# Performance work log

Measured on AMD Instinct MI355X. Metric: run time of the kernel, lower is better.

## Reference

```python
import jax, jax.numpy as jnp
import numpy as np

N_ATOMS = 8192
N_PAIR = 131072
F = 128
N_HEAD = 8
FH = F // N_HEAD            # 16
DEGREES = [1, 2, 3]
N_DEG = len(DEGREES)
REPEATS = np.array([2 * l + 1 for l in DEGREES])  # [3,5,7]
M_TOT = int(REPEATS.sum())  # 15
K_RBF = 32
H_FILT = 64
FILT_OUT = 2 * N_DEG * F    # 768


def setup_inputs() -> dict:
    key = jax.random.key(0)
    ks = jax.random.split(key, 12)
    x = jax.random.normal(ks[0], (N_ATOMS, F), dtype=jnp.float32)
    rbf_ij = jax.random.uniform(ks[1], (N_PAIR, K_RBF), dtype=jnp.float32)
    sph_ij = jax.random.normal(ks[2], (N_PAIR, M_TOT), dtype=jnp.float32)
    phi_r_cut = jax.random.uniform(ks[3], (N_PAIR,), dtype=jnp.float32)
    idx_i = jnp.sort(jax.random.randint(ks[4], (N_PAIR,), 0, N_ATOMS))
    idx_j = jax.random.randint(ks[5], (N_PAIR,), 0, N_ATOMS)
    pair_mask = jnp.ones((N_PAIR,), dtype=jnp.float32)
    # params (lecun-normal-ish scaling)
    W_Q = jax.random.normal(ks[6], (N_DEG, N_HEAD, FH, FH), dtype=jnp.float32) / np.sqrt(FH)
    W_K = jax.random.normal(ks[7], (N_DEG, N_HEAD, FH, FH), dtype=jnp.float32) / np.sqrt(FH)
    a = jax.random.normal(ks[8], (N_DEG, N_HEAD, 2 * FH), dtype=jnp.float32) / np.sqrt(2 * FH)
    mlp_w1 = jax.random.normal(ks[9], (K_RBF, H_FILT), dtype=jnp.float32) / np.sqrt(K_RBF)
    mlp_b1 = jnp.zeros((H_FILT,), dtype=jnp.float32)
    mlp_w2 = jax.random.normal(ks[10], (H_FILT, FILT_OUT), dtype=jnp.float32) / np.sqrt(H_FILT)
    mlp_b2 = jnp.zeros((FILT_OUT,), dtype=jnp.float32)
    return {"x": x, "rbf_ij": rbf_ij, "sph_ij": sph_ij, "phi_r_cut": phi_r_cut,
            "idx_i": idx_i, "idx_j": idx_j, "pair_mask": pair_mask,
            "W_Q": W_Q, "W_K": W_K, "a": a,
            "mlp_w1": mlp_w1, "mlp_b1": mlp_b1, "mlp_w2": mlp_w2, "mlp_b2": mlp_b2}


def reference(x, rbf_ij, sph_ij, phi_r_cut, idx_i, idx_j, pair_mask,
              W_Q, W_K, a, mlp_w1, mlp_b1, mlp_w2, mlp_b2):
    n = x.shape[0]
    x_head = x.reshape(n, N_HEAD, FH)                       # (n, h, fh)
    # per-atom, per-degree, per-head linear maps
    Q = jnp.einsum('dhij,nhj->ndhi', W_Q, x_head)           # (n, d, h, fh)
    K = jnp.einsum('dhij,nhj->ndhi', W_K, x_head)
    m4 = pair_mask[:, None, None, None]
    Q_i = Q[idx_i] * m4                                     # (p, d, h, fh)
    K_j = K[idx_j] * m4
    QK = jnp.concatenate((Q_i, K_j), axis=-1)               # (p, d, h, 2fh)
    # radial filter MLP
    h1 = jax.nn.silu(rbf_ij @ mlp_w1 + mlp_b1)
    W_ij = (h1 @ mlp_w2 + mlp_b2).reshape(-1, N_DEG, N_HEAD, 2 * FH)
    W_ij = W_ij * phi_r_cut[:, None, None, None]
    # attention logits (non-softmax)
    alpha = jnp.sum(QK * W_ij * a[None], axis=-1)           # (p, d, h)
    alpha = jnp.repeat(alpha, REPEATS, axis=1, total_repeat_length=M_TOT)  # (p, m, h)
    alpha = alpha / jnp.sqrt(jnp.float32(FH))               # att_scale
    # outer product with spherical harmonics + scatter
    x_j = x_head[idx_j] * pair_mask[:, None, None]          # (p, h, fh)
    z = alpha[..., None] * (sph_ij[:, :, None, None] * x_j[:, None, :, :])  # (p, m, h, fh)
    z = z.reshape(z.shape[0], M_TOT, F)                     # (p, m, F)
    return jax.ops.segment_sum(z, idx_i, num_segments=n)    # (n, m, F)
```

## Files before the change

kernel.cpp:

```cpp
#include <hip/hip_runtime.h>
#include <hip/hip_bf16.h>

#define N_ATOMS 8192
#define N_PAIR  131072
#define F       128
#define N_HEAD  8
#define FH      16
#define N_DEG   3
#define M_TOT   15
#define K_RBF   32
#define H_FILT  64
#define FILT_OUT 768
#define NDH     24

typedef __attribute__((ext_vector_type(8))) unsigned short u16x8;

__device__ __forceinline__ float bf2f(unsigned short u) {
    return __uint_as_float(((unsigned)u) << 16);
}
__device__ __forceinline__ unsigned short f2bfbits(float f) {
    __hip_bfloat16 b = __float2bfloat16(f);
    return *reinterpret_cast<unsigned short*>(&b);
}

__global__ void k_seg(const int* __restrict__ idx_i, int* __restrict__ row_start) {
    int p = blockIdx.x * 256 + threadIdx.x;
    if (p >= N_PAIR) return;
    int ii = idx_i[p];
    int prev = (p == 0) ? -1 : idx_i[p - 1];
    for (int a = prev + 1; a <= ii; ++a) row_start[a] = p;
    if (p == N_PAIR - 1) {
        for (int a = ii + 1; a <= N_ATOMS; ++a) row_start[a] = N_PAIR;
    }
}

__global__ void k_zero(int* __restrict__ counts, int* __restrict__ cnt2) {
    int t = blockIdx.x * 256 + threadIdx.x;
    if (t < N_ATOMS) { counts[t] = 0; cnt2[t] = 0; }
}

__global__ void k_hist(const int* __restrict__ idx_j, int* __restrict__ counts) {
    int p = blockIdx.x * 256 + threadIdx.x;
    if (p < N_PAIR) atomicAdd(&counts[idx_j[p]], 1);
}

__global__ __launch_bounds__(1024) void k_scan(const int* __restrict__ counts,
                                               int* __restrict__ offsets) {
    __shared__ int ts[1024];
    int tid = threadIdx.x;
    int base = tid * 8;
    int v[8]; int tot = 0;
    #pragma unroll
    for (int q = 0; q < 8; ++q) { v[q] = counts[base + q]; tot += v[q]; }
    ts[tid] = tot; __syncthreads();
    for (int off = 1; off < 1024; off <<= 1) {
        int t2 = (tid >= off) ? ts[tid - off] : 0;
        __syncthreads();
        ts[tid] += t2;
        __syncthreads();
    }
    int excl = ts[tid] - tot;
    #pragma unroll
    for (int q = 0; q < 8; ++q) { offsets[base + q] = excl; excl += v[q]; }
    if (tid == 1023) offsets[N_ATOMS] = ts[1023];
}

__global__ void k_place(const int* __restrict__ idx_j, const int* __restrict__ offsets,
                        int* __restrict__ cnt2, int* __restrict__ sorted,
                        int* __restrict__ rank) {
    int p = blockIdx.x * 256 + threadIdx.x;
    if (p < N_PAIR) {
        int j = idx_j[p];
        int pos = offsets[j] + atomicAdd(&cnt2[j], 1);
        sorted[pos] = p;
        rank[p] = pos;
    }
}

__global__ __launch_bounds__(256) void k_wc(
    const float* __restrict__ WQ, const float* __restrict__ WK,
    const float* __restrict__ avec, const float* __restrict__ W2,
    const float* __restrict__ b2,
    float* __restrict__ Wc, float* __restrict__ bc)
{
    int bx = blockIdx.x;
    int side = bx / NDH, dh = bx % NDH;
    int d = dh >> 3, h = dh & 7;
    int colbase = d * 256 + h * 32 + side * 16;
    const float* W = (side == 0) ? WQ : WK;
    __shared__ float w2s[64][16];
    __shared__ float ws[16][16];
    __shared__ float as[16];
    __shared__ float b2s[16];
    int tid = threadIdx.x;
    for (int e = tid; e < 64 * 16; e += 256)
        w2s[e >> 4][e & 15] = W2[(e >> 4) * FILT_OUT + colbase + (e & 15)];
    if (tid < 16 * 16) ws[tid >> 4][tid & 15] = W[((d * 8 + h) * 16) * 16 + tid];
    if (tid < 16) { as[tid] = avec[dh * 32 + side * 16 + tid]; b2s[tid] = b2[colbase + tid]; }
    __syncthreads();
    for (int o = tid; o < 64 * 16; o += 256) {
        int k = o >> 4, j = o & 15;
        float s = 0.f;
        #pragma unroll
        for (int c = 0; c < 16; ++c) s += w2s[k][c] * as[c] * ws[c][j];
        Wc[((size_t)bx * 64 + k) * 16 + j] = s;
    }
    if (tid < 16) {
        float s = 0.f;
        #pragma unroll
        for (int c = 0; c < 16; ++c) s += b2s[c] * as[c] * ws[c][tid];
        bc[bx * 16 + tid] = s;
    }
}

__global__ __launch_bounds__(256) void k_gfused(
    const float* __restrict__ x, const float* __restrict__ Wc,
    const float* __restrict__ bc,
    __hip_bfloat16* __restrict__ Gq, __hip_bfloat16* __restrict__ Gk,
    float* __restrict__ bq, float* __restrict__ bk)
{
    int bx = blockIdx.x;
    int by = blockIdx.y;
    int side = by / NDH, dh = by % NDH;
    int h = dh & 7;
    int n0 = bx * 64;
    __shared__ float xh[64][17];
    __shared__ float bcs[16];
    int tid = threadIdx.x;
    for (int e = tid; e < 64 * 16; e += 256)
        xh[e >> 4][e & 15] = x[(size_t)(n0 + (e >> 4)) * F + h * 16 + (e & 15)];
    if (tid < 16) bcs[tid] = bc[by * 16 + tid];
    int k = tid & 63, wv = tid >> 6;
    float wcr[16];
    const float* wp = Wc + ((size_t)by * 64 + k) * 16;
    #pragma unroll
    for (int j = 0; j < 16; ++j) wcr[j] = wp[j];
    __syncthreads();
    __hip_bfloat16* G = (side == 0) ? Gq : Gk;
    #pragma unroll 4
    for (int it = 0; it < 16; ++it) {
        int at = wv * 16 + it;
        float acc = 0.f;
        #pragma unroll
        for (int j = 0; j < 16; ++j) acc += wcr[j] * xh[at][j];
        G[(size_t)(n0 + at) * 1536 + dh * 64 + k] = __float2bfloat16(acc);
    }
    if (tid < 64) {
        float* B = (side == 0) ? bq : bk;
        float s = 0.f;
        #pragma unroll
        for (int j = 0; j < 16; ++j) s += bcs[j] * xh[tid][j];
        B[(n0 + tid) * NDH + dh] = s;
    }
}

__global__ __launch_bounds__(256) void k_h1(
    const float* __restrict__ rbf, const float* __restrict__ W1,
    const float* __restrict__ b1, unsigned short* __restrict__ h1)
{
    __shared__ float w1s[K_RBF][H_FILT];
    __shared__ float b1s[H_FILT];
    __shared__ float rbfs[64][33];
    int tid = threadIdx.x;
    int p0 = blockIdx.x * 64;
    for (int e = tid; e < K_RBF * H_FILT; e += 256) w1s[e >> 6][e & 63] = W1[e];
    if (tid < H_FILT) b1s[tid] = b1[tid];
    for (int e = tid; e < 64 * K_RBF; e += 256)
        rbfs[e >> 5][e & 31] = rbf[(size_t)p0 * K_RBF + e];
    __syncthreads();
    int pp = tid >> 2;
    int kbase = (tid & 3) * 16;
    float acc[16];
    #pragma unroll
    for (int q = 0; q < 16; ++q) acc[q] = b1s[kbase + q];
    for (int c = 0; c < K_RBF; ++c) {
        float r = rbfs[pp][c];
        #pragma unroll
        for (int q = 0; q < 16; ++q) acc[q] += r * w1s[c][kbase + q];
    }
    u16x8 o0, o1;
    #pragma unroll
    for (int q = 0; q < 8; ++q) {
        float s0 = acc[q];     o0[q] = f2bfbits(s0 / (1.f + __expf(-s0)));
        float s1 = acc[q + 8]; o1[q] = f2bfbits(s1 / (1.f + __expf(-s1)));
    }
    unsigned short* hp = h1 + (size_t)(p0 + pp) * 64 + kbase;
    *reinterpret_cast<u16x8*>(hp) = o0;
    *reinterpret_cast<u16x8*>(hp + 8) = o1;
}

__global__ __launch_bounds__(256) void k_alphak(
    const int* __restrict__ sorted, const int* __restrict__ idx_j,
    const unsigned short* __restrict__ h1,
    const __hip_bfloat16* __restrict__ Gk, const float* __restrict__ bk,
    unsigned short* __restrict__ alphaKs)
{
    __shared__ unsigned short h1s[64][64];
    __shared__ int ps[64];
    __shared__ int js[64];
    int tid = threadIdx.x;
    int c0 = blockIdx.x * 64;
    if (tid < 64) {
        int pid = sorted[c0 + tid];
        ps[tid] = pid;
        js[tid] = idx_j[pid];
    }
    __syncthreads();
    for (int e = tid; e < 64 * 8; e += 256) {
        int slot = e >> 3, seg = e & 7;
        *reinterpret_cast<u16x8*>(&h1s[slot][seg * 8]) =
            *reinterpret_cast<const u16x8*>(h1 + (size_t)ps[slot] * 64 + seg * 8);
    }
    __syncthreads();

    const unsigned short* GkU = reinterpret_cast<const unsigned short*>(Gk);
    unsigned sA, dA, sB, dB;
    const unsigned short* gA; const unsigned short* gB;
    float bkA, bkB;
    u16x8 vA[8], vB[8];

#define AK_ADDRLOAD(S, D, G, BK, V, T)                                   \
    { unsigned task = (T) * 256u + (unsigned)tid;                        \
      S = task / 24u; D = task - S * 24u;                                \
      int j_ = js[S];                                                    \
      G = GkU + (size_t)j_ * 1536 + D * 64;                              \
      BK = bk[j_ * NDH + D];                                             \
      _Pragma("unroll")                                                  \
      for (int v = 0; v < 8; ++v) V[v] = *reinterpret_cast<const u16x8*>(G + v * 8); }

#define AK_COMP(S, BK, V, T)                                             \
    { float a0 = 0.f, a1 = 0.f, a2 = 0.f, a3 = 0.f;                      \
      _Pragma("unroll")                                                  \
      for (int v = 0; v < 8; ++v) {                                      \
        u16x8 hv = *reinterpret_cast<const u16x8*>(&h1s[S][v * 8]);      \
        a0 += bf2f(V[v][0]) * bf2f(hv[0]);                               \
        a1 += bf2f(V[v][1]) * bf2f(hv[1]);                               \
        a2 += bf2f(V[v][2]) * bf2f(hv[2]);                               \
        a3 += bf2f(V[v][3]) * bf2f(hv[3]);                               \
        a0 += bf2f(V[v][4]) * bf2f(hv[4]);                               \
        a1 += bf2f(V[v][5]) * bf2f(hv[5]);                               \
        a2 += bf2f(V[v][6]) * bf2f(hv[6]);                               \
        a3 += bf2f(V[v][7]) * bf2f(hv[7]);                               \
      }                                                                  \
      alphaKs[(size_t)c0 * 24 + (T) * 256 + tid] =                       \
          f2bfbits(BK + (a0 + a1) + (a2 + a3)); }

    AK_ADDRLOAD(sA, dA, gA, bkA, vA, 0);
    AK_ADDRLOAD(sB, dB, gB, bkB, vB, 1); AK_COMP(sA, bkA, vA, 0);
    AK_ADDRLOAD(sA, dA, gA, bkA, vA, 2); AK_COMP(sB, bkB, vB, 1);
    AK_ADDRLOAD(sB, dB, gB, bkB, vB, 3); AK_COMP(sA, bkA, vA, 2);
    AK_ADDRLOAD(sA, dA, gA, bkA, vA, 4); AK_COMP(sB, bkB, vB, 3);
    AK_ADDRLOAD(sB, dB, gB, bkB, vB, 5); AK_COMP(sA, bkA, vA, 4);
    AK_COMP(sB, bkB, vB, 5);
#undef AK_ADDRLOAD
#undef AK_COMP
}

__global__ __launch_bounds__(256) void k_aggr3(
    const float* __restrict__ x, const float* __restrict__ sph,
    const float* __restrict__ phi, const float* __restrict__ mask,
    const int* __restrict__ idx_j, const int* __restrict__ rank,
    const unsigned short* __restrict__ h1,
    const __hip_bfloat16* __restrict__ Gq, const float* __restrict__ bq,
    const unsigned short* __restrict__ alphaKs,
    const int* __restrict__ row_start, float* __restrict__ out)
{
    int i = blockIdx.x;
    int tid = threadIdx.x;
    int f = tid & 127;
    int grp = tid >> 7;
    int h = f >> 4;

    __shared__ float xls[32][128];
    __shared__ unsigned short gqs[24][72];
    __shared__ unsigned short h1s[32][72];
    __shared__ float sls[32][15];
    __shared__ float als[32][24];
    __shared__ float bqs[24];
    __shared__ float pms[32];
    __shared__ float xms[32];
    __shared__ int rks[32];

    const unsigned short* gqrow = reinterpret_cast<const unsigned short*>(Gq) + (size_t)i * 1536;
    for (int e = tid; e < 24 * 64; e += 256) gqs[e >> 6][e & 63] = gqrow[e];
    if (tid < 24) bqs[tid] = bq[i * NDH + tid];
    int pstart = row_start[i], pend = row_start[i + 1];

    float acc[M_TOT];
    #pragma unroll
    for (int m = 0; m < M_TOT; ++m) acc[m] = 0.f;

    for (int pc = pstart; pc < pend; pc += 32) {
        int nb = min(32, pend - pc);
        __syncthreads();
        if (tid < nb) {
            int p = pc + tid;
            rks[tid] = rank[p];
            pms[tid] = phi[p] * mask[p] * 0.25f;
            xms[tid] = mask[p];
        }
        for (int e = tid; e < nb * 8; e += 256) {
            int q = e >> 3, seg = e & 7;
            *reinterpret_cast<u16x8*>(&h1s[q][seg * 8]) =
                *reinterpret_cast<const u16x8*>(h1 + (size_t)(pc + q) * 64 + seg * 8);
        }
        for (int e = tid; e < nb * M_TOT; e += 256)
            sls[e / M_TOT][e % M_TOT] = sph[(size_t)(pc + e / M_TOT) * M_TOT + e % M_TOT];
        for (int e = tid; e < nb * 32; e += 256) {
            int q = e >> 5, c4 = e & 31;
            int j = idx_j[pc + q];
            *reinterpret_cast<float4*>(&xls[q][c4 * 4]) =
                *reinterpret_cast<const float4*>(x + (size_t)j * F + c4 * 4);
        }
        __syncthreads();
        for (int e = tid; e < nb * 24; e += 256) {
            int q = e / 24, dh = e - q * 24;
            u16x8 qv[8];
            #pragma unroll
            for (int v = 0; v < 8; ++v) qv[v] = *reinterpret_cast<const u16x8*>(&gqs[dh][v * 8]);
            float aks = bf2f(alphaKs[(size_t)rks[q] * 24 + dh]);
            float a0 = 0.f, a1 = 0.f, a2 = 0.f, a3 = 0.f;
            #pragma unroll
            for (int v = 0; v < 8; ++v) {
                u16x8 hv = *reinterpret_cast<const u16x8*>(&h1s[q][v * 8]);
                a0 += bf2f(qv[v][0]) * bf2f(hv[0]);
                a1 += bf2f(qv[v][1]) * bf2f(hv[1]);
                a2 += bf2f(qv[v][2]) * bf2f(hv[2]);
                a3 += bf2f(qv[v][3]) * bf2f(hv[3]);
                a0 += bf2f(qv[v][4]) * bf2f(hv[4]);
                a1 += bf2f(qv[v][5]) * bf2f(hv[5]);
                a2 += bf2f(qv[v][6]) * bf2f(hv[6]);
                a3 += bf2f(qv[v][7]) * bf2f(hv[7]);
            }
            als[q][dh] = ((a0 + a1) + (a2 + a3) + bqs[dh] + aks) * pms[q];
        }
        __syncthreads();
        #pragma unroll
        for (int q2 = 0; q2 < 16; ++q2) {
            int q = q2 * 2 + grp;
            if (q < nb) {
                float xv = xls[q][f] * xms[q];
                float c0 = als[q][0 + h], c1 = als[q][8 + h], c2 = als[q][16 + h];
                #pragma unroll
                for (int m = 0; m < 3; ++m)  acc[m] += c0 * sls[q][m] * xv;
                #pragma unroll
                for (int m = 3; m < 8; ++m)  acc[m] += c1 * sls[q][m] * xv;
                #pragma unroll
                for (int m = 8; m < 15; ++m) acc[m] += c2 * sls[q][m] * xv;
            }
        }
    }
    __syncthreads();
    float* red = &xls[0][0];
    if (grp == 1) {
        #pragma unroll
        for (int m = 0; m < M_TOT; ++m) red[m * 128 + f] = acc[m];
    }
    __syncthreads();
    if (grp == 0) {
        size_t ob = (size_t)i * (M_TOT * F) + f;
        #pragma unroll
        for (int m = 0; m < M_TOT; ++m) out[ob + m * F] = acc[m] + red[m * 128 + f];
    }
}

extern "C" void kernel_launch(void* const* d_in, const int* in_sizes, int n_in,
                              void* d_out, int out_size, void* d_ws, size_t ws_size,
                              hipStream_t stream) {
    const float* x     = (const float*)d_in[0];
    const float* rbf   = (const float*)d_in[1];
    const float* sph   = (const float*)d_in[2];
    const float* phi   = (const float*)d_in[3];
    const int*   idx_i = (const int*)d_in[4];
    const int*   idx_j = (const int*)d_in[5];
    const float* mask  = (const float*)d_in[6];
    const float* WQ    = (const float*)d_in[7];
    const float* WK    = (const float*)d_in[8];
    const float* av    = (const float*)d_in[9];
    const float* W1    = (const float*)d_in[10];
    const float* b1    = (const float*)d_in[11];
    const float* W2    = (const float*)d_in[12];
    const float* b2    = (const float*)d_in[13];
    float* out = (float*)d_out;
    char* ws = (char*)d_ws;

    __hip_bfloat16* Gq = (__hip_bfloat16*)(ws + 0);
    __hip_bfloat16* Gk = (__hip_bfloat16*)(ws + 25165824);
    float* bq = (float*)(ws + 50331648);
    float* bk = (float*)(ws + 51118080);
    int* row_start = (int*)(ws + 51904512);
    int* counts    = (int*)(ws + 51937792);
    int* offsets   = (int*)(ws + 51970560);
    int* cnt2      = (int*)(ws + 52003840);
    int* sorted    = (int*)(ws + 52036608);
    int* rank      = (int*)(ws + 52560896);
    unsigned short* h1      = (unsigned short*)(ws + 53085184);
    unsigned short* alphaKs = (unsigned short*)(ws + 69862400);
    float* Wc = (float*)(ws + 76153856);
    float* bc = (float*)(ws + 76350464);

    k_zero<<<(N_ATOMS + 255) / 256, 256, 0, stream>>>(counts, cnt2);
    k_seg<<<(N_PAIR + 255) / 256, 256, 0, stream>>>(idx_i, row_start);
    k_hist<<<(N_PAIR + 255) / 256, 256, 0, stream>>>(idx_j, counts);
    k_scan<<<1, 1024, 0, stream>>>(counts, offsets);
    k_place<<<(N_PAIR + 255) / 256, 256, 0, stream>>>(idx_j, offsets, cnt2, sorted, rank);
    k_wc<<<48, 256, 0, stream>>>(WQ, WK, av, W2, b2, Wc, bc);
    k_gfused<<<dim3(N_ATOMS / 64, 48), 256, 0, stream>>>(x, Wc, bc, Gq, Gk, bq, bk);
    k_h1<<<N_PAIR / 64, 256, 0, stream>>>(rbf, W1, b1, h1);
    k_alphak<<<N_PAIR / 64, 256, 0, stream>>>(sorted, idx_j, h1, Gk, bk, alphaKs);
    k_aggr3<<<N_ATOMS, 256, 0, stream>>>(x, sph, phi, mask, idx_j, rank, h1, Gq, bq,
                                         alphaKs, row_start, out);
}
```

Measured before the change: 199.3 us.

## Split alpha-Q computation into separate pair-parallel kernel and batch atoms in aggregation

Moves the per-pair Q-side alpha dot product out of the per-atom aggregation kernel into a new pair-parallel kernel that writes fp32 alpha to workspace, reusing the Gk region after it is consumed. The aggregation kernel now handles 4 atoms per block, splits the 15 m-outputs across the two thread groups instead of doing a shared-memory reduction, and flushes accumulators whenever the atom index changes. The aim is to remove per-atom Gq staging and load imbalance from variable segment lengths. In exchange it adds a kernel launch and an extra round trip of the alpha array through global memory.

Result: slower. 233.6 us (+17.2%).

```diff
diff --git a/kernel.cpp b/kernel.cpp
--- a/kernel.cpp
+++ b/kernel.cpp
@@ -12,6 +12,7 @@
 #define H_FILT  64
 #define FILT_OUT 768
 #define NDH     24
+#define ATB     4
 
 typedef __attribute__((ext_vector_type(8))) unsigned short u16x8;
 
@@ -256,111 +257,181 @@
 #undef AK_COMP
 }
 
-__global__ __launch_bounds__(256) void k_aggr3(
-    const float* __restrict__ x, const float* __restrict__ sph,
+__global__ __launch_bounds__(256) void k_alphaA(
+    const int* __restrict__ idx_i, const int* __restrict__ rank,
     const float* __restrict__ phi, const float* __restrict__ mask,
-    const int* __restrict__ idx_j, const int* __restrict__ rank,
     const unsigned short* __restrict__ h1,
     const __hip_bfloat16* __restrict__ Gq, const float* __restrict__ bq,
     const unsigned short* __restrict__ alphaKs,
+    float* __restrict__ alphaF)
+{
+    __shared__ unsigned short h1s[64][64];
+    __shared__ int is[64];
+    __shared__ int rks[64];
+    __shared__ float pms[64];
+    int tid = threadIdx.x;
+    int p0 = blockIdx.x * 64;
+    if (tid < 64) {
+        int p = p0 + tid;
+        is[tid] = idx_i[p];
+        rks[tid] = rank[p];
+        pms[tid] = phi[p] * mask[p] * 0.25f;
+    }
+    __syncthreads();
+    for (int e = tid; e < 64 * 8; e += 256) {
+        int slot = e >> 3, seg = e & 7;
+        *reinterpret_cast<u16x8*>(&h1s[slot][seg * 8]) =
+            *reinterpret_cast<const u16x8*>(h1 + (size_t)(p0 + slot) * 64 + seg * 8);
+    }
+    __syncthreads();
+
+    const unsigned short* GqU = reinterpret_cast<const unsigned short*>(Gq);
+    unsigned sA, dA, sB, dB;
+    float baseA, baseB, pmA, pmB;
+    u16x8 vA[8], vB[8];
+
+#define QA_ADDRLOAD(S, D, BASE, PM, V, T)                                \
+    { unsigned task = (T) * 256u + (unsigned)tid;                        \
+      S = task / 24u; D = task - S * 24u;                                \
+      int i_ = is[S];                                                    \
+      const unsigned short* G = GqU + (size_t)i_ * 1536 + D * 64;        \
+      BASE = bq[i_ * NDH + D] + bf2f(alphaKs[(size_t)rks[S] * 24 + D]);  \
+      PM = pms[S];                                                       \
+      _Pragma("unroll")                                                  \
+      for (int v = 0; v < 8; ++v) V[v] = *reinterpret_cast<const u16x8*>(G + v * 8); }
+
+#define QA_COMP(S, BASE, PM, V, T)                                       \
+    { float a0 = 0.f, a1 = 0.f, a2 = 0.f, a3 = 0.f;                      \
+      _Pragma("unroll")                                                  \
+      for (int v = 0; v < 8; ++v) {                                      \
+        u16x8 hv = *reinterpret_cast<const u16x8*>(&h1s[S][v * 8]);      \
+        a0 += bf2f(V[v][0]) * bf2f(hv[0]);                               \
+        a1 += bf2f(V[v][1]) * bf2f(hv[1]);                               \
+        a2 += bf2f(V[v][2]) * bf2f(hv[2]);                               \
+        a3 += bf2f(V[v][3]) * bf2f(hv[3]);                               \
+        a0 += bf2f(V[v][4]) * bf2f(hv[4]);                               \
+        a1 += bf2f(V[v][5]) * bf2f(hv[5]);                               \
+        a2 += bf2f(V[v][6]) * bf2f(hv[6]);                               \
+        a3 += bf2f(V[v][7]) * bf2f(hv[7]);                               \
+      }                                                                  \
+      alphaF[(size_t)p0 * 24 + (T) * 256 + tid] =                        \
+          (BASE + (a0 + a1) + (a2 + a3)) * PM; }
+
+    QA_ADDRLOAD(sA, dA, baseA, pmA, vA, 0);
+    QA_ADDRLOAD(sB, dB, baseB, pmB, vB, 1); QA_COMP(sA, baseA, pmA, vA, 0);
+    QA_ADDRLOAD(sA, dA, baseA, pmA, vA, 2); QA_COMP(sB, baseB, pmB, vB, 1);
+    QA_ADDRLOAD(sB, dB, baseB, pmB, vB, 3); QA_COMP(sA, baseA, pmA, vA, 2);
+    QA_ADDRLOAD(sA, dA, baseA, pmA, vA, 4); QA_COMP(sB, baseB, pmB, vB, 3);
+    QA_ADDRLOAD(sB, dB, baseB, pmB, vB, 5); QA_COMP(sA, baseA, pmA, vA, 4);
+    QA_COMP(sB, baseB, pmB, vB, 5);
+#undef QA_ADDRLOAD
+#undef QA_COMP
+}
+
+__global__ __launch_bounds__(256) void k_aggr4(
+    const float* __restrict__ x, const float* __restrict__ sph,
+    const float* __restrict__ mask,
+    const int* __restrict__ idx_i, const int* __restrict__ idx_j,
+    const float* __restrict__ alphaF,
     const int* __restrict__ row_start, float* __restrict__ out)
 {
-    int i = blockIdx.x;
-    int tid = threadIdx.x;
-    int f = tid & 127;
-    int grp = tid >> 7;
-    int h = f >> 4;
+    int a0 = blockIdx.x * ATB;
+    int tid = threadIdx.x;
+    int f = tid & 127, grp = tid >> 7, h = f >> 4;
 
     __shared__ float xls[32][128];
-    __shared__ unsigned short gqs[24][72];
-    __shared__ unsigned short h1s[32][72];
+    __shared__ float als[32][24];
     __shared__ float sls[32][15];
-    __shared__ float als[32][24];
-    __shared__ float bqs[24];
-    __shared__ float pms[32];
+    __shared__ int   iis[32];
+    __shared__ int   jjs[32];
     __shared__ float xms[32];
-    __shared__ int rks[32];
-
-    const unsigned short* gqrow = reinterpret_cast<const unsigned short*>(Gq) + (size_t)i * 1536;
-    for (int e = tid; e < 24 * 64; e += 256) gqs[e >> 6][e & 63] = gqrow[e];
-    if (tid < 24) bqs[tid] = bq[i * NDH + tid];
-    int pstart = row_start[i], pend = row_start[i + 1];
-
-    float acc[M_TOT];
-    #pragma unroll
-    for (int m = 0; m < M_TOT; ++m) acc[m] = 0.f;
+    __shared__ int   rs[ATB + 1];
+
+    if (tid <= ATB) rs[tid] = row_start[a0 + tid];
+    __syncthreads();
+    int pstart = rs[0], pend = rs[ATB];
+
+    float acc[8];
+    #pragma unroll
+    for (int m = 0; m < 8; ++m) acc[m] = 0.f;
+    int cur = -1;
 
     for (int pc = pstart; pc < pend; pc += 32) {
         int nb = min(32, pend - pc);
         __syncthreads();
         if (tid < nb) {
             int p = pc + tid;
-            rks[tid] = rank[p];
-            pms[tid] = phi[p] * mask[p] * 0.25f;
+            iis[tid] = idx_i[p];
+            jjs[tid] = idx_j[p];
             xms[tid] = mask[p];
         }
-        for (int e = tid; e < nb * 8; e += 256) {
-            int q = e >> 3, seg = e & 7;
-            *reinterpret_cast<u16x8*>(&h1s[q][seg * 8]) =
-                *reinterpret_cast<const u16x8*>(h1 + (size_t)(pc + q) * 64 + seg * 8);
-        }
-        for (int e = tid; e < nb * M_TOT; e += 256)
-            sls[e / M_TOT][e % M_TOT] = sph[(size_t)(pc + e / M_TOT) * M_TOT + e % M_TOT];
+        for (int e = tid; e < nb * 24; e += 256)
+            als[e / 24][e % 24] = alphaF[(size_t)pc * 24 + e];
+        for (int e = tid; e < nb * 15; e += 256)
+            sls[e / 15][e % 15] = sph[(size_t)pc * 15 + e];
+        __syncthreads();
         for (int e = tid; e < nb * 32; e += 256) {
             int q = e >> 5, c4 = e & 31;
-            int j = idx_j[pc + q];
-            *reinterpret_cast<float4*>(&xls[q][c4 * 4]) =
-                *reinterpret_cast<const float4*>(x + (size_t)j * F + c4 * 4);
+            float4 v = *reinterpret_cast<const float4*>(x + (size_t)jjs[q] * F + c4 * 4);
+            float m_ = xms[q];
+            v.x *= m_; v.y *= m_; v.z *= m_; v.w *= m_;
+            *reinterpret_cast<float4*>(&xls[q][c4 * 4]) = v;
         }
         __syncthreads();
-        for (int e = tid; e < nb * 24; e += 256) {
-            int q = e / 24, dh = e - q * 24;
-            u16x8 qv[8];
-            #pragma unroll
-            for (int v = 0; v < 8; ++v) qv[v] = *reinterpret_cast<const u16x8*>(&gqs[dh][v * 8]);
-            float aks = bf2f(alphaKs[(size_t)rks[q] * 24 + dh]);
-            float a0 = 0.f, a1 = 0.f, a2 = 0.f, a3 = 0.f;
-            #pragma unroll
-            for (int v = 0; v < 8; ++v) {
-                u16x8 hv = *reinterpret_cast<const u16x8*>(&h1s[q][v * 8]);
-                a0 += bf2f(qv[v][0]) * bf2f(hv[0]);
-                a1 += bf2f(qv[v][1]) * bf2f(hv[1]);
-                a2 += bf2f(qv[v][2]) * bf2f(hv[2]);
-                a3 += bf2f(qv[v][3]) * bf2f(hv[3]);
-                a0 += bf2f(qv[v][4]) * bf2f(hv[4]);
-                a1 += bf2f(qv[v][5]) * bf2f(hv[5]);
-                a2 += bf2f(qv[v][6]) * bf2f(hv[6]);
-                a3 += bf2f(qv[v][7]) * bf2f(hv[7]);
+        for (int q = 0; q < nb; ++q) {
+            int ia = iis[q];
+            if (ia != cur) {
+                if (cur >= 0) {
+                    size_t ob = (size_t)cur * (M_TOT * F) + f;
+                    if (grp == 0) {
+                        #pragma unroll
+                        for (int m = 0; m < 8; ++m) out[ob + m * 128] = acc[m];
+                    } else {
+                        #pragma unroll
+                        for (int m = 0; m < 7; ++m) out[ob + (8 + m) * 128] = acc[m];
+                    }
+                }
+                cur = ia;
+                #pragma unroll
+                for (int m = 0; m < 8; ++m) acc[m] = 0.f;
             }
-            als[q][dh] = ((a0 + a1) + (a2 + a3) + bqs[dh] + aks) * pms[q];
-        }
-        __syncthreads();
-        #pragma unroll
-        for (int q2 = 0; q2 < 16; ++q2) {
-            int q = q2 * 2 + grp;
-            if (q < nb) {
-                float xv = xls[q][f] * xms[q];
-                float c0 = als[q][0 + h], c1 = als[q][8 + h], c2 = als[q][16 + h];
+            float xv = xls[q][f];
+            if (grp == 0) {
+                float t0 = als[q][h] * xv;
+                float t1 = als[q][8 + h] * xv;
+                acc[0] += t0 * sls[q][0];
+                acc[1] += t0 * sls[q][1];
+                acc[2] += t0 * sls[q][2];
                 #pragma unroll
-                for (int m = 0; m < 3; ++m)  acc[m] += c0 * sls[q][m] * xv;
+                for (int m = 3; m < 8; ++m) acc[m] += t1 * sls[q][m];
+            } else {
+                float t2 = als[q][16 + h] * xv;
                 #pragma unroll
-                for (int m = 3; m < 8; ++m)  acc[m] += c1 * sls[q][m] * xv;
-                #pragma unroll
-                for (int m = 8; m < 15; ++m) acc[m] += c2 * sls[q][m] * xv;
+                for (int m = 0; m < 7; ++m) acc[m] += t2 * sls[q][8 + m];
             }
         }
     }
-    __syncthreads();
-    float* red = &xls[0][0];
-    if (grp == 1) {
-        #pragma unroll
-        for (int m = 0; m < M_TOT; ++m) red[m * 128 + f] = acc[m];
-    }
-    __syncthreads();
-    if (grp == 0) {
-        size_t ob = (size_t)i * (M_TOT * F) + f;
-        #pragma unroll
-        for (int m = 0; m < M_TOT; ++m) out[ob + m * F] = acc[m] + red[m * 128 + f];
+    if (cur >= 0) {
+        size_t ob = (size_t)cur * (M_TOT * F) + f;
+        if (grp == 0) {
+            #pragma unroll
+            for (int m = 0; m < 8; ++m) out[ob + m * 128] = acc[m];
+        } else {
+            #pragma unroll
+            for (int m = 0; m < 7; ++m) out[ob + (8 + m) * 128] = acc[m];
+        }
+    }
+    for (int a = 0; a < ATB; ++a) {
+        if (rs[a] == rs[a + 1]) {
+            size_t ob = (size_t)(a0 + a) * (M_TOT * F) + f;
+            if (grp == 0) {
+                #pragma unroll
+                for (int m = 0; m < 8; ++m) out[ob + m * 128] = 0.f;
+            } else {
+                #pragma unroll
+                for (int m = 0; m < 7; ++m) out[ob + (8 + m) * 128] = 0.f;
+            }
+        }
     }
 }
 
@@ -386,6 +457,7 @@
 
     __hip_bfloat16* Gq = (__hip_bfloat16*)(ws + 0);
     __hip_bfloat16* Gk = (__hip_bfloat16*)(ws + 25165824);
+    float* alphaF = (float*)(ws + 25165824);
     float* bq = (float*)(ws + 50331648);
     float* bk = (float*)(ws + 51118080);
     int* row_start = (int*)(ws + 51904512);
@@ -408,6 +480,8 @@
     k_gfused<<<dim3(N_ATOMS / 64, 48), 256, 0, stream>>>(x, Wc, bc, Gq, Gk, bq, bk);
     k_h1<<<N_PAIR / 64, 256, 0, stream>>>(rbf, W1, b1, h1);
     k_alphak<<<N_PAIR / 64, 256, 0, stream>>>(sorted, idx_j, h1, Gk, bk, alphaKs);
-    k_aggr3<<<N_ATOMS, 256, 0, stream>>>(x, sph, phi, mask, idx_j, rank, h1, Gq, bq,
-                                         alphaKs, row_start, out);
-}
+    k_alphaA<<<N_PAIR / 64, 256, 0, stream>>>(idx_i, rank, phi, mask, h1, Gq, bq,
+                                              alphaKs, alphaF);
+    k_aggr4<<<N_ATOMS / ATB, 256, 0, stream>>>(x, sph, mask, idx_i, idx_j, alphaF,
+                                               row_start, out);
+}
```
